# Optimization experiments

Hardware: AMD Instinct MI355X
Metric: run time of the kernel (lower is better)

The kernel has to match this reference:

```python
import jax, jax.numpy as jnp
import numpy as np

N, E, G = 50000, 800000, 64          # nodes, edges, graphs in batch
H, C = 4, 32                          # heads, per-head channels
D = H * C                             # 128 = gat_hidden_dim * n_heads
EMB = 16
IN_DIM = 2 * EMB + 1                  # 33
LSTM_H = 256
OUT = 4
V_LAB, V_TYP = 1000, 100
EPS = 1e-5


def _gatv2(x, src, dst, Wl, bl, Wr, br, att, bias):
    # GATv2Conv (PyG semantics, self-loops already appended to src/dst).
    xl = (x @ Wl + bl).reshape(-1, H, C)   # lin_l -> source-side messages x_j
    xr = (x @ Wr + br).reshape(-1, H, C)   # lin_r -> target-side x_i
    xj = xl[src]                            # [Et, H, C]
    e = jax.nn.leaky_relu(xr[dst] + xj, 0.2)
    score = jnp.einsum('ehc,hc->eh', e, att)             # [Et, H]
    smax = jax.ops.segment_max(score, dst, num_segments=N)
    a = jnp.exp(score - smax[dst])
    denom = jax.ops.segment_sum(a, dst, num_segments=N)
    alpha = a / denom[dst]                                # scatter-softmax per dst
    out = jax.ops.segment_sum(xj * alpha[:, :, None], dst, num_segments=N)
    return out.reshape(N, D) + bias


def _graph_norm(x, batch_ids, w, b, ms):
    # PyG GraphNorm: per-graph mean (scaled by learnable ms) and variance.
    cnt = jax.ops.segment_sum(jnp.ones((N,), x.dtype), batch_ids, num_segments=G)[:, None]
    mean = jax.ops.segment_sum(x, batch_ids, num_segments=G) / cnt
    out = x - mean[batch_ids] * ms
    var = jax.ops.segment_sum(out * out, batch_ids, num_segments=G) / cnt
    return w * out / jnp.sqrt(var + EPS)[batch_ids] + b


def _lstm0(x, Wih, Whh, bih, bhh):
    # Single LSTM time-step with h0 = c0 = 0: the Whh @ h0 term vanishes,
    # the forget gate multiplies c0 = 0.  Gate order (PyTorch): i, f, g, o.
    g = x @ Wih.T + bih + bhh
    i, f, gg, o = jnp.split(g, 4, axis=-1)
    c = jax.nn.sigmoid(i) * jnp.tanh(gg)
    return jax.nn.sigmoid(o) * jnp.tanh(c)


def setup_inputs() -> dict:
    key = jax.random.key(0)
    ks = jax.random.split(key, 32)
    rn = lambda k, s, sc=0.05: jax.random.normal(k, s, jnp.float32) * sc
    Z4 = LSTM_H * 4
    return {
        'node_labels': jax.random.randint(ks[0], (N,), 0, V_LAB, jnp.int32),
        'node_types': jax.random.randint(ks[1], (N,), 0, V_TYP, jnp.int32),
        'node_feat': jax.random.normal(ks[2], (N, 1), jnp.float32),
        'edge_index': jax.random.randint(ks[3], (2, E), 0, N, jnp.int32),
        'batch_ids': jnp.sort(jax.random.randint(ks[4], (N,), 0, G, jnp.int32)),
        'emb_label': rn(ks[5], (V_LAB, EMB), 1.0),
        'emb_type': rn(ks[6], (V_TYP, EMB), 1.0),
        'W_in': rn(ks[7], (IN_DIM, D)), 'b_in': jnp.zeros((D,), jnp.float32),
        'g1_Wl': rn(ks[8], (D, D)), 'g1_bl': jnp.zeros((D,), jnp.float32),
        'g1_Wr': rn(ks[9], (D, D)), 'g1_br': jnp.zeros((D,), jnp.float32),
        'g1_att': rn(ks[10], (H, C), 0.1), 'g1_bias': jnp.zeros((D,), jnp.float32),
        'gn1_w': jnp.ones((D,), jnp.float32), 'gn1_b': jnp.zeros((D,), jnp.float32),
        'gn1_ms': jnp.ones((D,), jnp.float32),
        'g2_Wl': rn(ks[11], (D, D)), 'g2_bl': jnp.zeros((D,), jnp.float32),
        'g2_Wr': rn(ks[12], (D, D)), 'g2_br': jnp.zeros((D,), jnp.float32),
        'g2_att': rn(ks[13], (H, C), 0.1), 'g2_bias': jnp.zeros((D,), jnp.float32),
        'gn2_w': jnp.ones((D,), jnp.float32), 'gn2_b': jnp.zeros((D,), jnp.float32),
        'gn2_ms': jnp.ones((D,), jnp.float32),
        'W_res': rn(ks[14], (D, D)), 'b_res': jnp.zeros((D,), jnp.float32),
        'l1_Wih': rn(ks[15], (Z4, D)), 'l1_Whh': rn(ks[16], (Z4, LSTM_H)),
        'l1_bih': jnp.zeros((Z4,), jnp.float32), 'l1_bhh': jnp.zeros((Z4,), jnp.float32),
        'l2_Wih': rn(ks[17], (Z4, LSTM_H)), 'l2_Whh': rn(ks[18], (Z4, LSTM_H)),
        'l2_bih': jnp.zeros((Z4,), jnp.float32), 'l2_bhh': jnp.zeros((Z4,), jnp.float32),
        'ln_w': jnp.ones((LSTM_H,), jnp.float32), 'ln_b': jnp.zeros((LSTM_H,), jnp.float32),
        'fc_W': rn(ks[19], (LSTM_H, OUT)), 'fc_b': jnp.zeros((OUT,), jnp.float32),
    }


def reference(node_labels, node_types, node_feat, edge_index, batch_ids,
              emb_label, emb_type, W_in, b_in,
              g1_Wl, g1_bl, g1_Wr, g1_br, g1_att, g1_bias, gn1_w, gn1_b, gn1_ms,
              g2_Wl, g2_bl, g2_Wr, g2_br, g2_att, g2_bias, gn2_w, gn2_b, gn2_ms,
              W_res, b_res,
              l1_Wih, l1_Whh, l1_bih, l1_bhh, l2_Wih, l2_Whh, l2_bih, l2_bhh,
              ln_w, ln_b, fc_W, fc_b):
    # Node features: [label_emb | type_emb | scalar]  -> [N, 33]
    feat = jnp.concatenate([emb_label[node_labels], emb_type[node_types], node_feat], axis=1)
    # PositionalEncoding at position 0 with odd d_model=33 adds exactly zeros (no-op).
    x = feat @ W_in + b_in                                  # [N, D]

    loops = jnp.arange(N, dtype=edge_index.dtype)           # GATv2Conv add_self_loops=True
    src = jnp.concatenate([edge_index[0], loops])
    dst = jnp.concatenate([edge_index[1], loops])

    x1 = jax.nn.elu(_graph_norm(_gatv2(x, src, dst, g1_Wl, g1_bl, g1_Wr, g1_br, g1_att, g1_bias),
                                batch_ids, gn1_w, gn1_b, gn1_ms))
    # dropout = identity in eval mode
    x2 = jax.nn.elu(_graph_norm(_gatv2(x1, src, dst, g2_Wl, g2_bl, g2_Wr, g2_br, g2_att, g2_bias),
                                batch_ids, gn2_w, gn2_b, gn2_ms) + x1 @ W_res + b_res)

    h1 = _lstm0(x2, l1_Wih, l1_Whh, l1_bih, l1_bhh)         # seq_len = 1 LSTM
    h2 = _lstm0(h1, l2_Wih, l2_Whh, l2_bih, l2_bhh)

    mu = h2.mean(-1, keepdims=True)
    var = ((h2 - mu) ** 2).mean(-1, keepdims=True)
    hn = ln_w * (h2 - mu) / jnp.sqrt(var + EPS) + ln_b      # LayerNorm

    cnt = jax.ops.segment_sum(jnp.ones((N,), hn.dtype), batch_ids, num_segments=G)[:, None]
    pooled = jax.ops.segment_sum(hn, batch_ids, num_segments=G) / cnt  # global_mean_pool
    return jax.nn.log_softmax(pooled @ fc_W + fc_b, axis=1)            # [G, OUT]
```

## Files before the change

### kernel.cpp

```cpp
#include <hip/hip_runtime.h>
#include <cstdint>
#include <cstddef>

#define DD 128
#define LSTMH 256
#define ZG 1024

typedef __attribute__((ext_vector_type(8))) short short8v;
typedef __attribute__((ext_vector_type(4))) float float4v;

static inline int cdiv_(int a, int b) { return (a + b - 1) / b; }

__device__ __forceinline__ float sigm_(float x) { return 1.f / (1.f + __expf(-x)); }
__device__ __forceinline__ float tanh_(float x) {
  float e = __expf(-2.f * fabsf(x));
  float r = (1.f - e) / (1.f + e);
  return copysignf(r, x);
}

__device__ __forceinline__ unsigned short f2bf(float f) {
  uint32_t u = __float_as_uint(f);
  u += 0x7fffu + ((u >> 16) & 1u);
  return (unsigned short)(u >> 16);
}
__device__ __forceinline__ uint32_t bfpack(float a, float b) {
  return (uint32_t)f2bf(a) | ((uint32_t)f2bf(b) << 16);
}
__device__ __forceinline__ float bflo(uint32_t u) { return __uint_as_float(u << 16); }
__device__ __forceinline__ float bfhi(uint32_t u) { return __uint_as_float(u & 0xffff0000u); }

__global__ void prep_all(const float* __restrict__ g1Wl, const float* __restrict__ g1Wr,
                         const float* __restrict__ g2Wl, const float* __restrict__ g2Wr,
                         const float* __restrict__ Wres, const float* __restrict__ l1Wih,
                         const float* __restrict__ l2Wih, const float* __restrict__ g1bl,
                         const float* __restrict__ g1br, const float* __restrict__ g2bl,
                         const float* __restrict__ g2br, const float* __restrict__ bres,
                         const float* __restrict__ l1bih, const float* __restrict__ l1bhh,
                         const float* __restrict__ l2bih, const float* __restrict__ l2bhh,
                         unsigned short* __restrict__ wcat1, unsigned short* __restrict__ wcat2,
                         unsigned short* __restrict__ wl1b, unsigned short* __restrict__ wl2b,
                         float* __restrict__ bcat1, float* __restrict__ bcat2,
                         float* __restrict__ bsum1, float* __restrict__ bsum2,
                         int* __restrict__ deg, int* __restrict__ cursor,
                         float* __restrict__ pooled, int Nn) {
  int i = blockIdx.x * 256 + threadIdx.x;
  if (i < 81920) {
    int seg = i >> 14, j = i & 16383;
    int m = j >> 7, k = j & 127;
    const float* src = (seg == 0) ? g1Wl : (seg == 1) ? g1Wr : (seg == 2) ? g2Wl
                       : (seg == 3) ? g2Wr : Wres;
    unsigned short* dst = (seg == 0) ? wcat1 : (seg == 1) ? wcat1 + 16384
                          : (seg == 2) ? wcat2 : (seg == 3) ? wcat2 + 16384 : wcat2 + 32768;
    dst[j] = f2bf(src[k * 128 + m]);
    return;
  }
  i -= 81920;
  if (i < 131072) { wl1b[i] = f2bf(l1Wih[i]); return; }
  i -= 131072;
  if (i < 262144) { wl2b[i] = f2bf(l2Wih[i]); return; }
  i -= 262144;
  if (i < 256) { bcat1[i] = (i < 128) ? g1bl[i] : g1br[i - 128]; return; }
  i -= 256;
  if (i < 384) {
    bcat2[i] = (i < 128) ? g2bl[i] : (i < 256 ? g2br[i - 128] : bres[i - 256]);
    return;
  }
  i -= 384;
  if (i < 1024) { bsum1[i] = l1bih[i] + l1bhh[i]; return; }
  i -= 1024;
  if (i < 1024) { bsum2[i] = l2bih[i] + l2bhh[i]; return; }
  i -= 1024;
  if (i < Nn) { deg[i] = 0; return; }
  i -= Nn;
  if (i < Nn) { cursor[i] = 0; return; }
  i -= Nn;
  if (i < 16384) { pooled[i] = 0.f; return; }
}

__global__ __launch_bounds__(256) void embed_in2(
    const int* __restrict__ labels, const int* __restrict__ types,
    const float* __restrict__ nf, const float* __restrict__ embL,
    const float* __restrict__ embT, const float* __restrict__ W,
    const float* __restrict__ b, unsigned short* __restrict__ x, int N) {
  __shared__ float f[128][34];
  int base = blockIdx.x * 128;
  int tid = threadIdx.x;
  int ch = tid & 127, half = tid >> 7;
  float wr[33];
#pragma unroll
  for (int k = 0; k < 33; ++k) wr[k] = W[k * 128 + ch];
  float bb = b[ch];
  int nmax = N - base < 128 ? N - base : 128;
  for (int e = tid; e < nmax * 32; e += 256) {
    int n = e >> 5, k = e & 31;
    f[n][k] = (k < 16) ? embL[labels[base + n] * 16 + k] : embT[types[base + n] * 16 + (k - 16)];
  }
  for (int n = tid; n < nmax; n += 256) f[n][32] = nf[base + n];
  __syncthreads();
  for (int n = half; n < nmax; n += 2) {
    float acc = bb;
#pragma unroll
    for (int k = 0; k < 33; ++k) acc = fmaf(f[n][k], wr[k], acc);
    x[(size_t)(base + n) * 128 + ch] = f2bf(acc);
  }
}

__global__ void count_deg(const int* __restrict__ ei, int* __restrict__ deg, int E_, int N_) {
  int i = blockIdx.x * 256 + threadIdx.x;
  if (i < E_) atomicAdd(&deg[ei[E_ + i]], 1);
  else if (i < E_ + N_) atomicAdd(&deg[i - E_], 1);
}

__global__ __launch_bounds__(256) void scan1(const int* __restrict__ deg, int* __restrict__ offs,
                                             int* __restrict__ partials, int N_) {
  __shared__ int buf[2][256];
  int tid = threadIdx.x;
  int i = blockIdx.x * 256 + tid;
  int v = (i < N_) ? deg[i] : 0;
  buf[0][tid] = v;
  __syncthreads();
  int cur = 0;
#pragma unroll
  for (int d = 1; d < 256; d <<= 1) {
    int xv = buf[cur][tid];
    if (tid >= d) xv += buf[cur][tid - d];
    buf[cur ^ 1][tid] = xv;
    cur ^= 1;
    __syncthreads();
  }
  int incl = buf[cur][tid];
  if (i < N_) offs[i] = incl - v;
  if (tid == 255) partials[blockIdx.x] = incl;
}

__global__ __launch_bounds__(256) void scan2(int* __restrict__ partials, int* __restrict__ offs,
                                             int nb, int N_) {
  __shared__ int buf[2][256];
  int tid = threadIdx.x;
  int v = (tid < nb) ? partials[tid] : 0;
  buf[0][tid] = v;
  __syncthreads();
  int cur = 0;
#pragma unroll
  for (int d = 1; d < 256; d <<= 1) {
    int xv = buf[cur][tid];
    if (tid >= d) xv += buf[cur][tid - d];
    buf[cur ^ 1][tid] = xv;
    cur ^= 1;
    __syncthreads();
  }
  int incl = buf[cur][tid];
  if (tid < nb) partials[tid] = incl - v;
  if (tid == 255) offs[N_] = incl;
}

__global__ void scan3(int* __restrict__ offs, const int* __restrict__ partials, int N_) {
  int i = blockIdx.x * 256 + threadIdx.x;
  if (i < N_) offs[i] += partials[blockIdx.x];
}

__global__ void fill_csr(const int* __restrict__ ei, const int* __restrict__ offs,
                         int* __restrict__ cursor, int* __restrict__ csr, int E_, int N_) {
  int i = blockIdx.x * 256 + threadIdx.x;
  int s, d;
  if (i < E_) { s = ei[i]; d = ei[E_ + i]; }
  else if (i < E_ + N_) { s = d = i - E_; }
  else return;
  int pos = offs[d] + atomicAdd(&cursor[d], 1);
  csr[pos] = s;
}

__global__ void graph_ranges(const int* __restrict__ bids, int* __restrict__ gstart,
                             float* __restrict__ invcnt, int N_, int G_) {
  int t = threadIdx.x;
  if (t <= G_) {
    int lo = 0, hi = N_;
    while (lo < hi) { int mid = (lo + hi) >> 1; if (bids[mid] < t) lo = mid + 1; else hi = mid; }
    gstart[t] = lo;
  }
  __syncthreads();
  if (t < G_) {
    int c = gstart[t + 1] - gstart[t];
    invcnt[t] = (c > 0) ? 1.f / (float)c : 0.f;
  }
}

__global__ __launch_bounds__(256) void gemm_bf16(
    const unsigned short* __restrict__ A, const unsigned short* __restrict__ Bp,
    const float* __restrict__ bias, unsigned short* __restrict__ C, int M, int K, int Ncols) {
  __shared__ unsigned short As[128 * 40];
  __shared__ unsigned short Bs[128 * 40];
  int tid = threadIdx.x;
  int lane = tid & 63;
  int wid = tid >> 6;
  int rowBase = blockIdx.y * 128, colBase = blockIdx.x * 128;
  int wr = (wid >> 1) * 64, wc = (wid & 1) * 64;
  int fr = lane & 15, fg = lane >> 4;
  float4v acc[4][4];
#pragma unroll
  for (int i = 0; i < 4; ++i)
#pragma unroll
    for (int j = 0; j < 4; ++j) acc[i][j] = (float4v){0.f, 0.f, 0.f, 0.f};

  int sr = tid >> 2;
  int sc = tid & 3;
  int off_lo = (sc < 2) ? 32 * sc : 32 * sc - 56;

  for (int k0 = 0; k0 < K; k0 += 32) {
#pragma unroll
    for (int it = 0; it < 2; ++it) {
      int r = it * 64 + sr;
      uint4 va = make_uint4(0u, 0u, 0u, 0u);
      if (rowBase + r < M)
        va = *(const uint4*)(A + (size_t)(rowBase + r) * K + k0 + sc * 8);
      char* arow = (char*)(As + r * 40);
      *(uint2*)(arow + off_lo) = make_uint2(va.x, va.y);
      *(uint2*)(arow + off_lo + 16) = make_uint2(va.z, va.w);
      uint4 vb = *(const uint4*)(Bp + (size_t)(colBase + r) * K + k0 + sc * 8);
      char* brow = (char*)(Bs + r * 40);
      *(uint2*)(brow + off_lo) = make_uint2(vb.x, vb.y);
      *(uint2*)(brow + off_lo + 16) = make_uint2(vb.z, vb.w);
    }
    __syncthreads();
    short8v af[4], bfv[4];
#pragma unroll
    for (int i = 0; i < 4; ++i)
      af[i] = *(const short8v*)((const char*)As + (wr + 16 * i + fr) * 80 + fg * 16);
#pragma unroll
    for (int j = 0; j < 4; ++j)
      bfv[j] = *(const short8v*)((const char*)Bs + (wc + 16 * j + fr) * 80 + fg * 16);
#pragma unroll
    for (int i = 0; i < 4; ++i)
#pragma unroll
      for (int j = 0; j < 4; ++j)
        acc[i][j] = __builtin_amdgcn_mfma_f32_16x16x32_bf16(af[i], bfv[j], acc[i][j], 0, 0, 0);
    __syncthreads();
  }
#pragma unroll
  for (int j = 0; j < 4; ++j) {
    int gc = colBase + wc + 16 * j + fr;
    float bv = bias[gc];
#pragma unroll
    for (int i = 0; i < 4; ++i) {
      int gr0 = rowBase + wr + 16 * i + fg * 4;
#pragma unroll
      for (int rg = 0; rg < 4; ++rg) {
        int gr = gr0 + rg;
        if (gr < M) C[(size_t)gr * Ncols + gc] = f2bf(acc[i][j][rg] + bv);
      }
    }
  }
}

__global__ __launch_bounds__(256) void gat_agg(
    const unsigned short* __restrict__ xlr, int stride,
    const int* __restrict__ csr, const int* __restrict__ offs,
    const float* __restrict__ att, const float* __restrict__ bias,
    unsigned short* __restrict__ out, float* __restrict__ gz, int N) {
  int zt = blockIdx.x * 256 + threadIdx.x;
  if (zt < 4096) *(float4*)(gz + zt * 4) = make_float4(0.f, 0.f, 0.f, 0.f);
  int wid = zt >> 6;
  if (wid >= N) return;
  int lane = threadIdx.x & 63;
  int q = lane >> 4, ql = lane & 15;
  float4 aA = *(const float4*)&att[ql * 8];
  float4 aB = *(const float4*)&att[ql * 8 + 4];
  uint4 ur = *(const uint4*)(xlr + (size_t)wid * stride + 128 + ql * 8);
  float r0 = bflo(ur.x), r1 = bfhi(ur.x), r2 = bflo(ur.y), r3 = bfhi(ur.y);
  float r4 = bflo(ur.z), r5 = bfhi(ur.z), r6 = bflo(ur.w), r7 = bfhi(ur.w);
  float m = -1e30f, L = 0.f;
  float s0 = 0.f, s1 = 0.f, s2 = 0.f, s3 = 0.f, s4 = 0.f, s5 = 0.f, s6 = 0.f, s7 = 0.f;
  int js = offs[wid], je = offs[wid + 1];
  for (int j = js + q; j < je; j += 4) {
    int s = csr[j];
    uint4 u = *(const uint4*)(xlr + (size_t)s * stride + ql * 8);
    float x0 = bflo(u.x), x1 = bfhi(u.x), x2 = bflo(u.y), x3 = bfhi(u.y);
    float x4 = bflo(u.z), x5 = bfhi(u.z), x6 = bflo(u.w), x7 = bfhi(u.w);
    float v0 = fmaxf(r0 + x0, 0.2f * (r0 + x0));
    float v1 = fmaxf(r1 + x1, 0.2f * (r1 + x1));
    float v2 = fmaxf(r2 + x2, 0.2f * (r2 + x2));
    float v3 = fmaxf(r3 + x3, 0.2f * (r3 + x3));
    float v4 = fmaxf(r4 + x4, 0.2f * (r4 + x4));
    float v5 = fmaxf(r5 + x5, 0.2f * (r5 + x5));
    float v6 = fmaxf(r6 + x6, 0.2f * (r6 + x6));
    float v7 = fmaxf(r7 + x7, 0.2f * (r7 + x7));
    float p = aA.x * v0 + aA.y * v1 + aA.z * v2 + aA.w * v3 +
              aB.x * v4 + aB.y * v5 + aB.z * v6 + aB.w * v7;
    p += __shfl_xor(p, 1); p += __shfl_xor(p, 2);
    float mn = fmaxf(m, p);
    float ea = __expf(p - mn);
    float es = __expf(m - mn);
    L = L * es + ea;
    s0 = s0 * es + ea * x0; s1 = s1 * es + ea * x1;
    s2 = s2 * es + ea * x2; s3 = s3 * es + ea * x3;
    s4 = s4 * es + ea * x4; s5 = s5 * es + ea * x5;
    s6 = s6 * es + ea * x6; s7 = s7 * es + ea * x7;
    m = mn;
  }
#pragma unroll
  for (int d = 16; d <= 32; d <<= 1) {
    float mo = __shfl_xor(m, d), Lo = __shfl_xor(L, d);
    float t0 = __shfl_xor(s0, d), t1 = __shfl_xor(s1, d);
    float t2 = __shfl_xor(s2, d), t3 = __shfl_xor(s3, d);
    float t4 = __shfl_xor(s4, d), t5 = __shfl_xor(s5, d);
    float t6 = __shfl_xor(s6, d), t7 = __shfl_xor(s7, d);
    float mn = fmaxf(m, mo);
    float e0 = __expf(m - mn), e1 = __expf(mo - mn);
    L = L * e0 + Lo * e1;
    s0 = s0 * e0 + t0 * e1; s1 = s1 * e0 + t1 * e1;
    s2 = s2 * e0 + t2 * e1; s3 = s3 * e0 + t3 * e1;
    s4 = s4 * e0 + t4 * e1; s5 = s5 * e0 + t5 * e1;
    s6 = s6 * e0 + t6 * e1; s7 = s7 * e0 + t7 * e1;
    m = mn;
  }
  if (q == 0) {
    float inv = 1.f / L;
    float4 bA = *(const float4*)&bias[ql * 8];
    float4 bB = *(const float4*)&bias[ql * 8 + 4];
    uint4 ov;
    ov.x = bfpack(s0 * inv + bA.x, s1 * inv + bA.y);
    ov.y = bfpack(s2 * inv + bA.z, s3 * inv + bA.w);
    ov.z = bfpack(s4 * inv + bB.x, s5 * inv + bB.y);
    ov.w = bfpack(s6 * inv + bB.z, s7 * inv + bB.w);
    *(uint4*)(out + (size_t)wid * DD + ql * 8) = ov;
  }
}

__global__ __launch_bounds__(256) void gn_stats2(const unsigned short* __restrict__ x,
                                                 const int* __restrict__ bids,
                                                 float* __restrict__ gsum,
                                                 float* __restrict__ gsq, int N) {
  int base = blockIdx.x * 128;
  int cp = threadIdx.x & 63;
  int sub = threadIdx.x >> 6;
  int end = base + 128 < N ? base + 128 : N;
  int curg = -1;
  float s0 = 0.f, s1 = 0.f, q0 = 0.f, q1 = 0.f;
  for (int r = base + sub; r < end; r += 4) {
    int g = bids[r];
    if (g != curg) {
      if (curg >= 0) {
        atomicAdd(&gsum[curg * DD + cp * 2], s0);
        atomicAdd(&gsum[curg * DD + cp * 2 + 1], s1);
        atomicAdd(&gsq[curg * DD + cp * 2], q0);
        atomicAdd(&gsq[curg * DD + cp * 2 + 1], q1);
      }
      curg = g; s0 = s1 = q0 = q1 = 0.f;
    }
    uint32_t u = *(const uint32_t*)(x + (size_t)r * DD + cp * 2);
    float v0 = bflo(u), v1 = bfhi(u);
    s0 += v0; q0 += v0 * v0; s1 += v1; q1 += v1 * v1;
  }
  if (curg >= 0) {
    atomicAdd(&gsum[curg * DD + cp * 2], s0);
    atomicAdd(&gsum[curg * DD + cp * 2 + 1], s1);
    atomicAdd(&gsq[curg * DD + cp * 2], q0);
    atomicAdd(&gsq[curg * DD + cp * 2 + 1], q1);
  }
}

template <bool ADDRES>
__global__ void gn_apply(const unsigned short* __restrict__ xin,
                         unsigned short* __restrict__ xout,
                         const unsigned short* __restrict__ res, int resStride,
                         const int* __restrict__ bids, const float* __restrict__ gsum,
                         const float* __restrict__ gsq, const float* __restrict__ invcnt,
                         const float* __restrict__ w, const float* __restrict__ b,
                         const float* __restrict__ ms, int N) {
  int idx = blockIdx.x * 256 + threadIdx.x;
  if (idx >= N * 64) return;
  int n = idx >> 6, cp = idx & 63;
  int g = bids[n];
  float ic = invcnt[g];
  float2 sm = *(const float2*)&gsum[g * DD + cp * 2];
  float2 sq = *(const float2*)&gsq[g * DD + cp * 2];
  float2 w2 = *(const float2*)&w[cp * 2];
  float2 b2 = *(const float2*)&b[cp * 2];
  float2 m2 = *(const float2*)&ms[cp * 2];
  uint32_t u = *(const uint32_t*)(xin + (size_t)n * DD + cp * 2);
  float mean0 = sm.x * ic, mean1 = sm.y * ic;
  float mm0 = mean0 * m2.x, mm1 = mean1 * m2.y;
  float var0 = sq.x * ic - mm0 * (2.f * mean0 - mm0);
  float var1 = sq.y * ic - mm1 * (2.f * mean1 - mm1);
  float v0 = (bflo(u) - mm0) * rsqrtf(var0 + 1e-5f) * w2.x + b2.x;
  float v1 = (bfhi(u) - mm1) * rsqrtf(var1 + 1e-5f) * w2.y + b2.y;
  if (ADDRES) {
    uint32_t ur = *(const uint32_t*)(res + (size_t)n * resStride + cp * 2);
    v0 += bflo(ur); v1 += bfhi(ur);
  }
  v0 = v0 > 0.f ? v0 : (__expf(v0) - 1.f);
  v1 = v1 > 0.f ? v1 : (__expf(v1) - 1.f);
  *(uint32_t*)(xout + (size_t)n * DD + cp * 2) = bfpack(v0, v1);
}

template <int KD>
__global__ __launch_bounds__(512, 6) void lstm_big(
    const unsigned short* __restrict__ A, const unsigned short* __restrict__ Bp,
    const float* __restrict__ bsum, unsigned short* __restrict__ H, int M) {
  __shared__ __attribute__((aligned(16))) char As_[128 * 136];
  __shared__ __attribute__((aligned(16))) char Ws_[96 * 136];
  const int NPH = KD / 64;
  int npanel = (M + 127) >> 7;
  int b = blockIdx.x;
  int g8 = b & 7, inner = b >> 3;
  int p = g8 + 8 * (inner >> 3);
  int cc = inner & 7;
  if (p >= npanel) return;
  int rowBase = p << 7;
  int ch0 = cc * 32;

  int tid = threadIdx.x;
  int lane = tid & 63;
  int wid = tid >> 6;
  int wr4 = wid >> 1;
  int wc2 = wid & 1;
  int fr = lane & 15, fg = lane >> 4;

  int aldst[2], agoff[2];
  bool aval[2];
#pragma unroll
  for (int q = 0; q < 2; ++q) {
    int e = q * 512 + tid;
    int r = e >> 3, kk = e & 7;
    int c = kk >> 2, sc = kk & 3;
    int olo = (sc < 2) ? 32 * sc : 32 * sc - 56;
    aldst[q] = r * 136 + c * 64 + olo;
    aval[q] = (rowBase + r) < M;
    agoff[q] = (rowBase + r) * KD + c * 32 + sc * 8;
  }
  bool wact1 = tid < 256;
  int wldst[2], wgoff[2];
#pragma unroll
  for (int q = 0; q < 2; ++q) {
    int e = q * 512 + tid;
    int wrow = e >> 3, kk = e & 7;
    int c = kk >> 2, sc = kk & 3;
    int half = wrow >= 48 ? 1 : 0;
    int r3 = wrow - 48 * half;
    int grp = r3 >> 4;
    int goff = (grp == 0) ? 0 : (grp == 1 ? 512 : 768);
    int grow = goff + ch0 + 16 * half + (r3 & 15);
    int olo = (sc < 2) ? 32 * sc : 32 * sc - 56;
    wldst[q] = wrow * 136 + c * 64 + olo;
    wgoff[q] = grow * KD + c * 32 + sc * 8;
  }

  float4v acc[2][3];
#pragma unroll
  for (int i = 0; i < 2; ++i)
#pragma unroll
    for (int j = 0; j < 3; ++j) acc[i][j] = (float4v){0.f, 0.f, 0.f, 0.f};

  uint4 va[2], vw[2];
#pragma unroll
  for (int q = 0; q < 2; ++q) {
    va[q] = make_uint4(0u, 0u, 0u, 0u);
    if (aval[q]) va[q] = *(const uint4*)(A + agoff[q]);
  }
  vw[0] = *(const uint4*)(Bp + wgoff[0]);
  if (wact1) vw[1] = *(const uint4*)(Bp + wgoff[1]);

#pragma unroll
  for (int ph = 0; ph < NPH; ++ph) {
    if (ph) __syncthreads();
#pragma unroll
    for (int q = 0; q < 2; ++q) {
      char* dst = As_ + aldst[q];
      *(uint2*)(dst) = make_uint2(va[q].x, va[q].y);
      *(uint2*)(dst + 16) = make_uint2(va[q].z, va[q].w);
    }
    {
      char* dst = Ws_ + wldst[0];
      *(uint2*)(dst) = make_uint2(vw[0].x, vw[0].y);
      *(uint2*)(dst + 16) = make_uint2(vw[0].z, vw[0].w);
    }
    if (wact1) {
      char* dst = Ws_ + wldst[1];
      *(uint2*)(dst) = make_uint2(vw[1].x, vw[1].y);
      *(uint2*)(dst + 16) = make_uint2(vw[1].z, vw[1].w);
    }
    __syncthreads();
    if (ph + 1 < NPH) {
      int koff = (ph + 1) * 64;
#pragma unroll
      for (int q = 0; q < 2; ++q) {
        va[q] = make_uint4(0u, 0u, 0u, 0u);
        if (aval[q]) va[q] = *(const uint4*)(A + agoff[q] + koff);
      }
      vw[0] = *(const uint4*)(Bp + wgoff[0] + koff);
      if (wact1) vw[1] = *(const uint4*)(Bp + wgoff[1] + koff);
    }
    __builtin_amdgcn_s_setprio(1);
#pragma unroll
    for (int c = 0; c < 2; ++c) {
      short8v af[2], bf[3];
#pragma unroll
      for (int i = 0; i < 2; ++i)
        af[i] = *(const short8v*)(As_ + (32 * wr4 + 16 * i + fr) * 136 + c * 64 + fg * 16);
#pragma unroll
      for (int j = 0; j < 3; ++j)
        bf[j] = *(const short8v*)(Ws_ + (48 * wc2 + 16 * j + fr) * 136 + c * 64 + fg * 16);
#pragma unroll
      for (int i = 0; i < 2; ++i)
#pragma unroll
        for (int j = 0; j < 3; ++j)
          acc[i][j] = __builtin_amdgcn_mfma_f32_16x16x32_bf16(af[i], bf[j], acc[i][j], 0, 0, 0);
    }
    __builtin_amdgcn_s_setprio(0);
  }
  int chL = 16 * wc2 + fr;
  int ch = ch0 + chL;
  float bi = bsum[ch], bg = bsum[512 + ch], bo = bsum[768 + ch];
  unsigned short hv[8];
#pragma unroll
  for (int i = 0; i < 2; ++i) {
#pragma unroll
    for (int rg = 0; rg < 4; ++rg) {
      float iv = acc[i][0][rg] + bi;
      float gv = acc[i][1][rg] + bg;
      float ov = acc[i][2][rg] + bo;
      float c = sigm_(iv) * tanh_(gv);
      hv[i * 4 + rg] = f2bf(sigm_(ov) * tanh_(c));
    }
  }
  __syncthreads();
  unsigned short* Hs = (unsigned short*)As_;
#pragma unroll
  for (int i = 0; i < 2; ++i) {
#pragma unroll
    for (int rg = 0; rg < 4; ++rg) {
      int row = 32 * wr4 + 16 * i + 4 * fg + rg;
      Hs[row * 40 + chL] = hv[i * 4 + rg];
    }
  }
  __syncthreads();
  {
    int row = tid >> 2, seg = tid & 3;
    if (rowBase + row < M) {
      uint4 v = *(const uint4*)(Hs + row * 40 + seg * 8);
      *(uint4*)(H + (size_t)(rowBase + row) * LSTMH + ch0 + seg * 8) = v;
    }
  }
}

__global__ __launch_bounds__(256) void ln_pool2(
    const unsigned short* __restrict__ h2, const int* __restrict__ bids,
    const float* __restrict__ lnw, const float* __restrict__ lnb,
    const float* __restrict__ invcnt, float* __restrict__ pooled, int N) {
  int wave = (blockIdx.x * 256 + threadIdx.x) >> 6;
  int lane = threadIdx.x & 63;
  int r0 = wave * 8;
  if (r0 >= N) return;
  float4 w4 = *(const float4*)&lnw[lane * 4];
  float4 b4 = *(const float4*)&lnb[lane * 4];
  float p0 = 0.f, p1 = 0.f, p2 = 0.f, p3 = 0.f;
  int curg = bids[r0];
  int rend = r0 + 8 < N ? r0 + 8 : N;
  for (int r = r0; r < rend; ++r) {
    int g = bids[r];
    if (g != curg) {
      float ic = invcnt[curg];
      atomicAdd(&pooled[curg * LSTMH + lane * 4 + 0], p0 * ic);
      atomicAdd(&pooled[curg * LSTMH + lane * 4 + 1], p1 * ic);
      atomicAdd(&pooled[curg * LSTMH + lane * 4 + 2], p2 * ic);
      atomicAdd(&pooled[curg * LSTMH + lane * 4 + 3], p3 * ic);
      p0 = p1 = p2 = p3 = 0.f;
      curg = g;
    }
    uint2 u = *(const uint2*)(h2 + (size_t)r * LSTMH + lane * 4);
    float v0 = bflo(u.x), v1 = bfhi(u.x), v2 = bflo(u.y), v3 = bfhi(u.y);
    float s = v0 + v1 + v2 + v3;
    float q = v0 * v0 + v1 * v1 + v2 * v2 + v3 * v3;
#pragma unroll
    for (int d = 1; d < 64; d <<= 1) { s += __shfl_xor(s, d); q += __shfl_xor(q, d); }
    float mu = s * (1.f / 256.f);
    float var = q * (1.f / 256.f) - mu * mu;
    float rs = rsqrtf(var + 1e-5f);
    p0 += w4.x * (v0 - mu) * rs + b4.x;
    p1 += w4.y * (v1 - mu) * rs + b4.y;
    p2 += w4.z * (v2 - mu) * rs + b4.z;
    p3 += w4.w * (v3 - mu) * rs + b4.w;
  }
  float ic = invcnt[curg];
  atomicAdd(&pooled[curg * LSTMH + lane * 4 + 0], p0 * ic);
  atomicAdd(&pooled[curg * LSTMH + lane * 4 + 1], p1 * ic);
  atomicAdd(&pooled[curg * LSTMH + lane * 4 + 2], p2 * ic);
  atomicAdd(&pooled[curg * LSTMH + lane * 4 + 3], p3 * ic);
}

__global__ __launch_bounds__(64) void fc_lsm(const float* __restrict__ pooled,
                                             const float* __restrict__ W,
                                             const float* __restrict__ b, float* __restrict__ out) {
  int g = blockIdx.x;
  int t = threadIdx.x;
  float l0 = 0.f, l1 = 0.f, l2 = 0.f, l3 = 0.f;
  for (int k = t; k < LSTMH; k += 64) {
    float p = pooled[g * LSTMH + k];
    l0 += p * W[k * 4 + 0];
    l1 += p * W[k * 4 + 1];
    l2 += p * W[k * 4 + 2];
    l3 += p * W[k * 4 + 3];
  }
#pragma unroll
  for (int d = 1; d < 64; d <<= 1) {
    l0 += __shfl_xor(l0, d); l1 += __shfl_xor(l1, d);
    l2 += __shfl_xor(l2, d); l3 += __shfl_xor(l3, d);
  }
  if (t == 0) {
    float z[4] = {l0 + b[0], l1 + b[1], l2 + b[2], l3 + b[3]};
    float mx = fmaxf(fmaxf(z[0], z[1]), fmaxf(z[2], z[3]));
    float sum = __expf(z[0] - mx) + __expf(z[1] - mx) + __expf(z[2] - mx) + __expf(z[3] - mx);
    float ls = logf(sum);
#pragma unroll
    for (int o = 0; o < 4; ++o) out[g * 4 + o] = z[o] - mx - ls;
  }
}

extern "C" void kernel_launch(void* const* d_in, const int* in_sizes, int n_in,
                              void* d_out, int out_size, void* d_ws, size_t ws_size,
                              hipStream_t stream) {
  const int* node_labels = (const int*)d_in[0];
  const int* node_types = (const int*)d_in[1];
  const float* node_feat = (const float*)d_in[2];
  const int* edge_index = (const int*)d_in[3];
  const int* batch_ids = (const int*)d_in[4];
  const float* emb_label = (const float*)d_in[5];
  const float* emb_type = (const float*)d_in[6];
  const float* W_in = (const float*)d_in[7];
  const float* b_in = (const float*)d_in[8];
  const float* g1_Wl = (const float*)d_in[9];
  const float* g1_bl = (const float*)d_in[10];
  const float* g1_Wr = (const float*)d_in[11];
  const float* g1_br = (const float*)d_in[12];
  const float* g1_att = (const float*)d_in[13];
  const float* g1_bias = (const float*)d_in[14];
  const float* gn1_w = (const float*)d_in[15];
  const float* gn1_b = (const float*)d_in[16];
  const float* gn1_ms = (const float*)d_in[17];
  const float* g2_Wl = (const float*)d_in[18];
  const float* g2_bl = (const float*)d_in[19];
  const float* g2_Wr = (const float*)d_in[20];
  const float* g2_br = (const float*)d_in[21];
  const float* g2_att = (const float*)d_in[22];
  const float* g2_bias = (const float*)d_in[23];
  const float* gn2_w = (const float*)d_in[24];
  const float* gn2_b = (const float*)d_in[25];
  const float* gn2_ms = (const float*)d_in[26];
  const float* W_res = (const float*)d_in[27];
  const float* b_res = (const float*)d_in[28];
  const float* l1_Wih = (const float*)d_in[29];
  const float* l1_bih = (const float*)d_in[31];
  const float* l1_bhh = (const float*)d_in[32];
  const float* l2_Wih = (const float*)d_in[33];
  const float* l2_bih = (const float*)d_in[35];
  const float* l2_bhh = (const float*)d_in[36];
  const float* ln_w = (const float*)d_in[37];
  const float* ln_b = (const float*)d_in[38];
  const float* fc_W = (const float*)d_in[39];
  const float* fc_b = (const float*)d_in[40];
  float* out = (float*)d_out;

  const int N = in_sizes[0];
  const int E = in_sizes[3] / 2;
  const int G = out_size / 4;
  const int ET = E + N;

  char* wsb = (char*)d_ws;
  size_t off = 0;
  auto alloc = [&](size_t bytes) -> void* {
    void* p = (void*)(wsb + off);
    off = (off + bytes + 255) & ~(size_t)255;
    return p;
  };
  unsigned short* xA = (unsigned short*)alloc((size_t)N * 512);
  unsigned short* xb = (unsigned short*)alloc((size_t)N * DD * 2);
  unsigned short* xlr = (unsigned short*)alloc((size_t)N * 384 * 2);
  int* deg = (int*)alloc((size_t)N * 4);
  int* offs = (int*)alloc((size_t)(N + 1) * 4);
  int* cursor = (int*)alloc((size_t)N * 4);
  int* partials = (int*)alloc(1024);
  int* csr = (int*)alloc((size_t)ET * 4);
  int* gstart = (int*)alloc((size_t)(G + 1) * 4);
  float* invcnt = (float*)alloc((size_t)G * 4);
  float* gsum = (float*)alloc((size_t)G * DD * 4);
  float* gsq = (float*)alloc((size_t)G * DD * 4);
  float* pooled = (float*)alloc((size_t)G * LSTMH * 4);
  float* bcat1 = (float*)alloc(256 * 4);
  float* bcat2 = (float*)alloc(384 * 4);
  float* bsum1 = (float*)alloc(ZG * 4);
  float* bsum2 = (float*)alloc(ZG * 4);
  unsigned short* wcat1 = (unsigned short*)alloc((size_t)256 * DD * 2);
  unsigned short* wcat2 = (unsigned short*)alloc((size_t)384 * DD * 2);
  unsigned short* wl1b = (unsigned short*)alloc((size_t)ZG * DD * 2);
  unsigned short* wl2b = (unsigned short*)alloc((size_t)ZG * LSTMH * 2);
  (void)ws_size; (void)n_in;

  unsigned short* h1 = xlr;
  unsigned short* h2 = xA;

  int prepTotal = 477824 + 2 * N + 16384;
  prep_all<<<cdiv_(prepTotal, 256), 256, 0, stream>>>(
      g1_Wl, g1_Wr, g2_Wl, g2_Wr, W_res, l1_Wih, l2_Wih,
      g1_bl, g1_br, g2_bl, g2_br, b_res, l1_bih, l1_bhh, l2_bih, l2_bhh,
      wcat1, wcat2, wl1b, wl2b, bcat1, bcat2, bsum1, bsum2,
      deg, cursor, pooled, N);
  graph_ranges<<<1, 128, 0, stream>>>(batch_ids, gstart, invcnt, N, G);
  embed_in2<<<cdiv_(N, 128), 256, 0, stream>>>(node_labels, node_types, node_feat, emb_label,
                                               emb_type, W_in, b_in, xb, N);

  count_deg<<<cdiv_(ET, 256), 256, 0, stream>>>(edge_index, deg, E, N);
  int nb1 = cdiv_(N, 256);
  scan1<<<nb1, 256, 0, stream>>>(deg, offs, partials, N);
  scan2<<<1, 256, 0, stream>>>(partials, offs, nb1, N);
  scan3<<<nb1, 256, 0, stream>>>(offs, partials, N);
  fill_csr<<<cdiv_(ET, 256), 256, 0, stream>>>(edge_index, offs, cursor, csr, E, N);

  int mb = cdiv_(N, 128);
  gemm_bf16<<<dim3(2, mb), 256, 0, stream>>>(xb, wcat1, bcat1, xlr, N, DD, 256);
  gat_agg<<<cdiv_(N, 4), 256, 0, stream>>>(xlr, 256, csr, offs, g1_att, g1_bias, xA, gsum, N);
  gn_stats2<<<cdiv_(N, 128), 256, 0, stream>>>(xA, batch_ids, gsum, gsq, N);
  gn_apply<false><<<cdiv_(N * 64, 256), 256, 0, stream>>>(
      xA, xb, nullptr, 0, batch_ids, gsum, gsq, invcnt, gn1_w, gn1_b, gn1_ms, N);
  gemm_bf16<<<dim3(3, mb), 256, 0, stream>>>(xb, wcat2, bcat2, xlr, N, DD, 384);
  gat_agg<<<cdiv_(N, 4), 256, 0, stream>>>(xlr, 384, csr, offs, g2_att, g2_bias, xA, gsum, N);
  gn_stats2<<<cdiv_(N, 128), 256, 0, stream>>>(xA, batch_ids, gsum, gsq, N);
  gn_apply<true><<<cdiv_(N * 64, 256), 256, 0, stream>>>(
      xA, xb, xlr + 256, 384, batch_ids, gsum, gsq, invcnt, gn2_w, gn2_b, gn2_ms, N);
  int npanel = cdiv_(N, 128);
  int lblocks = 64 * cdiv_(npanel, 8);
  lstm_big<DD><<<lblocks, 512, 0, stream>>>(xb, wl1b, bsum1, h1, N);
  lstm_big<LSTMH><<<lblocks, 512, 0, stream>>>(h1, wl2b, bsum2, h2, N);
  ln_pool2<<<cdiv_(N, 32), 256, 0, stream>>>(h2, batch_ids, ln_w, ln_b, invcnt, pooled, N);
  fc_lsm<<<G, 64, 0, stream>>>(pooled, fc_W, fc_b, out);
}
```

Before: 476.7 us.

## Widen GAT lanes to 16 channels and shrink LSTM blocks to 4 waves

In the GAT aggregation kernel, each lane now handles 16 channels instead of 8, so 8 edges are processed in parallel per wave instead of 4. This halves the per-edge score shuffle reduction and adds one cross-group merge stage. The LSTM GEMM kernel moves from 512 to 256 threads per block, with each wave computing a 64x48 tile (4x3 MFMA fragments) instead of 32x48. This increases per-wave register use and reuse of the B fragments, while trading away occupancy and latency hiding.

```diff
diff --git a/kernel.cpp b/kernel.cpp
--- a/kernel.cpp
+++ b/kernel.cpp
@@ -262,67 +262,75 @@
   int wid = zt >> 6;
   if (wid >= N) return;
   int lane = threadIdx.x & 63;
-  int q = lane >> 4, ql = lane & 15;
-  float4 aA = *(const float4*)&att[ql * 8];
-  float4 aB = *(const float4*)&att[ql * 8 + 4];
-  uint4 ur = *(const uint4*)(xlr + (size_t)wid * stride + 128 + ql * 8);
-  float r0 = bflo(ur.x), r1 = bfhi(ur.x), r2 = bflo(ur.y), r3 = bfhi(ur.y);
-  float r4 = bflo(ur.z), r5 = bfhi(ur.z), r6 = bflo(ur.w), r7 = bfhi(ur.w);
+  int q = lane >> 3, ql = lane & 7;
+  float4 aA = *(const float4*)&att[ql * 16];
+  float4 aB = *(const float4*)&att[ql * 16 + 4];
+  float4 aC = *(const float4*)&att[ql * 16 + 8];
+  float4 aD = *(const float4*)&att[ql * 16 + 12];
+  uint4 urA = *(const uint4*)(xlr + (size_t)wid * stride + 128 + ql * 16);
+  uint4 urB = *(const uint4*)(xlr + (size_t)wid * stride + 128 + ql * 16 + 8);
+  float r[16] = {bflo(urA.x), bfhi(urA.x), bflo(urA.y), bfhi(urA.y),
+                 bflo(urA.z), bfhi(urA.z), bflo(urA.w), bfhi(urA.w),
+                 bflo(urB.x), bfhi(urB.x), bflo(urB.y), bfhi(urB.y),
+                 bflo(urB.z), bfhi(urB.z), bflo(urB.w), bfhi(urB.w)};
+  float am[16] = {aA.x, aA.y, aA.z, aA.w, aB.x, aB.y, aB.z, aB.w,
+                  aC.x, aC.y, aC.z, aC.w, aD.x, aD.y, aD.z, aD.w};
   float m = -1e30f, L = 0.f;
-  float s0 = 0.f, s1 = 0.f, s2 = 0.f, s3 = 0.f, s4 = 0.f, s5 = 0.f, s6 = 0.f, s7 = 0.f;
+  float s[16];
+#pragma unroll
+  for (int c = 0; c < 16; ++c) s[c] = 0.f;
   int js = offs[wid], je = offs[wid + 1];
-  for (int j = js + q; j < je; j += 4) {
-    int s = csr[j];
-    uint4 u = *(const uint4*)(xlr + (size_t)s * stride + ql * 8);
-    float x0 = bflo(u.x), x1 = bfhi(u.x), x2 = bflo(u.y), x3 = bfhi(u.y);
-    float x4 = bflo(u.z), x5 = bfhi(u.z), x6 = bflo(u.w), x7 = bfhi(u.w);
-    float v0 = fmaxf(r0 + x0, 0.2f * (r0 + x0));
-    float v1 = fmaxf(r1 + x1, 0.2f * (r1 + x1));
-    float v2 = fmaxf(r2 + x2, 0.2f * (r2 + x2));
-    float v3 = fmaxf(r3 + x3, 0.2f * (r3 + x3));
-    float v4 = fmaxf(r4 + x4, 0.2f * (r4 + x4));
-    float v5 = fmaxf(r5 + x5, 0.2f * (r5 + x5));
-    float v6 = fmaxf(r6 + x6, 0.2f * (r6 + x6));
-    float v7 = fmaxf(r7 + x7, 0.2f * (r7 + x7));
-    float p = aA.x * v0 + aA.y * v1 + aA.z * v2 + aA.w * v3 +
-              aB.x * v4 + aB.y * v5 + aB.z * v6 + aB.w * v7;
-    p += __shfl_xor(p, 1); p += __shfl_xor(p, 2);
+  for (int j = js + q; j < je; j += 8) {
+    int sn = csr[j];
+    uint4 uA = *(const uint4*)(xlr + (size_t)sn * stride + ql * 16);
+    uint4 uB = *(const uint4*)(xlr + (size_t)sn * stride + ql * 16 + 8);
+    float x[16] = {bflo(uA.x), bfhi(uA.x), bflo(uA.y), bfhi(uA.y),
+                   bflo(uA.z), bfhi(uA.z), bflo(uA.w), bfhi(uA.w),
+                   bflo(uB.x), bfhi(uB.x), bflo(uB.y), bfhi(uB.y),
+                   bflo(uB.z), bfhi(uB.z), bflo(uB.w), bfhi(uB.w)};
+    float p = 0.f;
+#pragma unroll
+    for (int c = 0; c < 16; ++c) {
+      float v = r[c] + x[c];
+      v = fmaxf(v, 0.2f * v);
+      p = fmaf(am[c], v, p);
+    }
+    p += __shfl_xor(p, 1);
     float mn = fmaxf(m, p);
     float ea = __expf(p - mn);
     float es = __expf(m - mn);
     L = L * es + ea;
-    s0 = s0 * es + ea * x0; s1 = s1 * es + ea * x1;
-    s2 = s2 * es + ea * x2; s3 = s3 * es + ea * x3;
-    s4 = s4 * es + ea * x4; s5 = s5 * es + ea * x5;
-    s6 = s6 * es + ea * x6; s7 = s7 * es + ea * x7;
+#pragma unroll
+    for (int c = 0; c < 16; ++c) s[c] = fmaf(ea, x[c], s[c] * es);
     m = mn;
   }
 #pragma unroll
-  for (int d = 16; d <= 32; d <<= 1) {
+  for (int d = 8; d <= 32; d <<= 1) {
     float mo = __shfl_xor(m, d), Lo = __shfl_xor(L, d);
-    float t0 = __shfl_xor(s0, d), t1 = __shfl_xor(s1, d);
-    float t2 = __shfl_xor(s2, d), t3 = __shfl_xor(s3, d);
-    float t4 = __shfl_xor(s4, d), t5 = __shfl_xor(s5, d);
-    float t6 = __shfl_xor(s6, d), t7 = __shfl_xor(s7, d);
+    float t[16];
+#pragma unroll
+    for (int c = 0; c < 16; ++c) t[c] = __shfl_xor(s[c], d);
     float mn = fmaxf(m, mo);
     float e0 = __expf(m - mn), e1 = __expf(mo - mn);
     L = L * e0 + Lo * e1;
-    s0 = s0 * e0 + t0 * e1; s1 = s1 * e0 + t1 * e1;
-    s2 = s2 * e0 + t2 * e1; s3 = s3 * e0 + t3 * e1;
-    s4 = s4 * e0 + t4 * e1; s5 = s5 * e0 + t5 * e1;
-    s6 = s6 * e0 + t6 * e1; s7 = s7 * e0 + t7 * e1;
+#pragma unroll
+    for (int c = 0; c < 16; ++c) s[c] = s[c] * e0 + t[c] * e1;
     m = mn;
   }
   if (q == 0) {
     float inv = 1.f / L;
-    float4 bA = *(const float4*)&bias[ql * 8];
-    float4 bB = *(const float4*)&bias[ql * 8 + 4];
-    uint4 ov;
-    ov.x = bfpack(s0 * inv + bA.x, s1 * inv + bA.y);
-    ov.y = bfpack(s2 * inv + bA.z, s3 * inv + bA.w);
-    ov.z = bfpack(s4 * inv + bB.x, s5 * inv + bB.y);
-    ov.w = bfpack(s6 * inv + bB.z, s7 * inv + bB.w);
-    *(uint4*)(out + (size_t)wid * DD + ql * 8) = ov;
+    uint4 o1, o2;
+    const float* bp = &bias[ql * 16];
+    o1.x = bfpack(s[0] * inv + bp[0], s[1] * inv + bp[1]);
+    o1.y = bfpack(s[2] * inv + bp[2], s[3] * inv + bp[3]);
+    o1.z = bfpack(s[4] * inv + bp[4], s[5] * inv + bp[5]);
+    o1.w = bfpack(s[6] * inv + bp[6], s[7] * inv + bp[7]);
+    o2.x = bfpack(s[8] * inv + bp[8], s[9] * inv + bp[9]);
+    o2.y = bfpack(s[10] * inv + bp[10], s[11] * inv + bp[11]);
+    o2.z = bfpack(s[12] * inv + bp[12], s[13] * inv + bp[13]);
+    o2.w = bfpack(s[14] * inv + bp[14], s[15] * inv + bp[15]);
+    *(uint4*)(out + (size_t)wid * DD + ql * 16) = o1;
+    *(uint4*)(out + (size_t)wid * DD + ql * 16 + 8) = o2;
   }
 }
 
@@ -394,7 +402,7 @@
 }
 
 template <int KD>
-__global__ __launch_bounds__(512, 6) void lstm_big(
+__global__ __launch_bounds__(256, 4) void lstm_big(
     const unsigned short* __restrict__ A, const unsigned short* __restrict__ Bp,
     const float* __restrict__ bsum, unsigned short* __restrict__ H, int M) {
   __shared__ __attribute__((aligned(16))) char As_[128 * 136];
@@ -412,15 +420,15 @@
   int tid = threadIdx.x;
   int lane = tid & 63;
   int wid = tid >> 6;
-  int wr4 = wid >> 1;
+  int wr2 = wid >> 1;
   int wc2 = wid & 1;
   int fr = lane & 15, fg = lane >> 4;
 
-  int aldst[2], agoff[2];
-  bool aval[2];
-#pragma unroll
-  for (int q = 0; q < 2; ++q) {
-    int e = q * 512 + tid;
+  int aldst[4], agoff[4];
+  bool aval[4];
+#pragma unroll
+  for (int q = 0; q < 4; ++q) {
+    int e = q * 256 + tid;
     int r = e >> 3, kk = e & 7;
     int c = kk >> 2, sc = kk & 3;
     int olo = (sc < 2) ? 32 * sc : 32 * sc - 56;
@@ -428,11 +436,10 @@
     aval[q] = (rowBase + r) < M;
     agoff[q] = (rowBase + r) * KD + c * 32 + sc * 8;
   }
-  bool wact1 = tid < 256;
-  int wldst[2], wgoff[2];
-#pragma unroll
-  for (int q = 0; q < 2; ++q) {
-    int e = q * 512 + tid;
+  int wldst[3], wgoff[3];
+#pragma unroll
+  for (int q = 0; q < 3; ++q) {
+    int e = q * 256 + tid;
     int wrow = e >> 3, kk = e & 7;
     int c = kk >> 2, sc = kk & 3;
     int half = wrow >= 48 ? 1 : 0;
@@ -445,63 +452,59 @@
     wgoff[q] = grow * KD + c * 32 + sc * 8;
   }
 
-  float4v acc[2][3];
-#pragma unroll
-  for (int i = 0; i < 2; ++i)
+  float4v acc[4][3];
+#pragma unroll
+  for (int i = 0; i < 4; ++i)
 #pragma unroll
     for (int j = 0; j < 3; ++j) acc[i][j] = (float4v){0.f, 0.f, 0.f, 0.f};
 
-  uint4 va[2], vw[2];
-#pragma unroll
-  for (int q = 0; q < 2; ++q) {
+  uint4 va[4], vw[3];
+#pragma unroll
+  for (int q = 0; q < 4; ++q) {
     va[q] = make_uint4(0u, 0u, 0u, 0u);
     if (aval[q]) va[q] = *(const uint4*)(A + agoff[q]);
   }
-  vw[0] = *(const uint4*)(Bp + wgoff[0]);
-  if (wact1) vw[1] = *(const uint4*)(Bp + wgoff[1]);
+#pragma unroll
+  for (int q = 0; q < 3; ++q) vw[q] = *(const uint4*)(Bp + wgoff[q]);
 
 #pragma unroll
   for (int ph = 0; ph < NPH; ++ph) {
     if (ph) __syncthreads();
 #pragma unroll
-    for (int q = 0; q < 2; ++q) {
+    for (int q = 0; q < 4; ++q) {
       char* dst = As_ + aldst[q];
       *(uint2*)(dst) = make_uint2(va[q].x, va[q].y);
       *(uint2*)(dst + 16) = make_uint2(va[q].z, va[q].w);
     }
-    {
-      char* dst = Ws_ + wldst[0];
-      *(uint2*)(dst) = make_uint2(vw[0].x, vw[0].y);
-      *(uint2*)(dst + 16) = make_uint2(vw[0].z, vw[0].w);
-    }
-    if (wact1) {
-      char* dst = Ws_ + wldst[1];
-      *(uint2*)(dst) = make_uint2(vw[1].x, vw[1].y);
-      *(uint2*)(dst + 16) = make_uint2(vw[1].z, vw[1].w);
+#pragma unroll
+    for (int q = 0; q < 3; ++q) {
+      char* dst = Ws_ + wldst[q];
+      *(uint2*)(dst) = make_uint2(vw[q].x, vw[q].y);
+      *(uint2*)(dst + 16) = make_uint2(vw[q].z, vw[q].w);
     }
     __syncthreads();
     if (ph + 1 < NPH) {
       int koff = (ph + 1) * 64;
 #pragma unroll
-      for (int q = 0; q < 2; ++q) {
+      for (int q = 0; q < 4; ++q) {
         va[q] = make_uint4(0u, 0u, 0u, 0u);
         if (aval[q]) va[q] = *(const uint4*)(A + agoff[q] + koff);
       }
-      vw[0] = *(const uint4*)(Bp + wgoff[0] + koff);
-      if (wact1) vw[1] = *(const uint4*)(Bp + wgoff[1] + koff);
+#pragma unroll
+      for (int q = 0; q < 3; ++q) vw[q] = *(const uint4*)(Bp + wgoff[q] + koff);
     }
     __builtin_amdgcn_s_setprio(1);
 #pragma unroll
     for (int c = 0; c < 2; ++c) {
-      short8v af[2], bf[3];
-#pragma unroll
-      for (int i = 0; i < 2; ++i)
-        af[i] = *(const short8v*)(As_ + (32 * wr4 + 16 * i + fr) * 136 + c * 64 + fg * 16);
+      short8v af[4], bf[3];
+#pragma unroll
+      for (int i = 0; i < 4; ++i)
+        af[i] = *(const short8v*)(As_ + (64 * wr2 + 16 * i + fr) * 136 + c * 64 + fg * 16);
 #pragma unroll
       for (int j = 0; j < 3; ++j)
         bf[j] = *(const short8v*)(Ws_ + (48 * wc2 + 16 * j + fr) * 136 + c * 64 + fg * 16);
 #pragma unroll
-      for (int i = 0; i < 2; ++i)
+      for (int i = 0; i < 4; ++i)
 #pragma unroll
         for (int j = 0; j < 3; ++j)
           acc[i][j] = __builtin_amdgcn_mfma_f32_16x16x32_bf16(af[i], bf[j], acc[i][j], 0, 0, 0);
@@ -511,9 +514,9 @@
   int chL = 16 * wc2 + fr;
   int ch = ch0 + chL;
   float bi = bsum[ch], bg = bsum[512 + ch], bo = bsum[768 + ch];
-  unsigned short hv[8];
-#pragma unroll
-  for (int i = 0; i < 2; ++i) {
+  unsigned short hv[16];
+#pragma unroll
+  for (int i = 0; i < 4; ++i) {
 #pragma unroll
     for (int rg = 0; rg < 4; ++rg) {
       float iv = acc[i][0][rg] + bi;
@@ -526,16 +529,18 @@
   __syncthreads();
   unsigned short* Hs = (unsigned short*)As_;
 #pragma unroll
-  for (int i = 0; i < 2; ++i) {
+  for (int i = 0; i < 4; ++i) {
 #pragma unroll
     for (int rg = 0; rg < 4; ++rg) {
-      int row = 32 * wr4 + 16 * i + 4 * fg + rg;
+      int row = 64 * wr2 + 16 * i + 4 * fg + rg;
       Hs[row * 40 + chL] = hv[i * 4 + rg];
     }
   }
   __syncthreads();
-  {
-    int row = tid >> 2, seg = tid & 3;
+#pragma unroll
+  for (int q = 0; q < 2; ++q) {
+    int e = q * 256 + tid;
+    int row = e >> 2, seg = e & 3;
     if (rowBase + row < M) {
       uint4 v = *(const uint4*)(Hs + row * 40 + seg * 8);
       *(uint4*)(H + (size_t)(rowBase + row) * LSTMH + ch0 + seg * 8) = v;
@@ -728,8 +733,8 @@
       xA, xb, xlr + 256, 384, batch_ids, gsum, gsq, invcnt, gn2_w, gn2_b, gn2_ms, N);
   int npanel = cdiv_(N, 128);
   int lblocks = 64 * cdiv_(npanel, 8);
-  lstm_big<DD><<<lblocks, 512, 0, stream>>>(xb, wl1b, bsum1, h1, N);
-  lstm_big<LSTMH><<<lblocks, 512, 0, stream>>>(h1, wl2b, bsum2, h2, N);
+  lstm_big<DD><<<lblocks, 256, 0, stream>>>(xb, wl1b, bsum1, h1, N);
+  lstm_big<LSTMH><<<lblocks, 256, 0, stream>>>(h1, wl2b, bsum2, h2, N);
   ln_pool2<<<cdiv_(N, 32), 256, 0, stream>>>(h2, batch_ids, ln_w, ln_b, invcnt, pooled, N);
   fc_lsm<<<G, 64, 0, stream>>>(pooled, fc_W, fc_b, out);
 }
```

Result: slower. 512.7 us (+7.6%).
